# Performance work log

Hardware: AMD Instinct MI355X
Metric: run time of the kernel (lower is better)

## Reference

```python
import jax, jax.numpy as jnp
import numpy as np
import math

# dims
B, C, T, P = 32, 8, 20000, 25          # batch, emg channels, time, patch size
D, H, M, NL = 512, 8, 256, 2            # d_model, heads, random features, layers
FFN, NC, HID = 1024, 10, 128            # ffn hidden, num classes, pool hidden
DH = D // H                             # d_head
EPS_LN = 1e-5


def _sample_omega(d, m, rng):
    # Orthogonal Random Features: blocks of QR(G) rows scaled by chi(d) norms
    blocks = []
    for _ in range(math.ceil(m / d)):
        G = rng.standard_normal((d, d)).astype(np.float32)
        Q, _ = np.linalg.qr(G)
        S = Q * np.linalg.norm(G, axis=1, keepdims=True)
        blocks.append(S.T)
    return np.concatenate(blocks, axis=1)[:, :m]


def setup_inputs() -> dict:
    key = jax.random.key(0)
    ks = jax.random.split(key, 16)
    rng = np.random.default_rng(0)
    s = 0.02
    f32 = jnp.float32
    return {
        "x": jax.random.normal(ks[0], (B, C, T), f32),
        "patch_W": jax.random.normal(ks[1], (C * P, D), f32) * s,
        "patch_b": jnp.zeros((D,), f32),
        "patch_g": jnp.ones((D,), f32),
        "patch_beta": jnp.zeros((D,), f32),
        "ln1_g": jnp.ones((NL, D), f32),
        "ln1_b": jnp.zeros((NL, D), f32),
        "qW": jax.random.normal(ks[2], (NL, D, D), f32) * s,
        "kW": jax.random.normal(ks[3], (NL, D, D), f32) * s,
        "vW": jax.random.normal(ks[4], (NL, D, D), f32) * s,
        "oW": jax.random.normal(ks[5], (NL, D, D), f32) * s,
        "ob": jnp.zeros((NL, D), f32),
        "omega": jnp.stack([jnp.asarray(_sample_omega(DH, M, rng)) for _ in range(NL)]),
        "ln2_g": jnp.ones((NL, D), f32),
        "ln2_b": jnp.zeros((NL, D), f32),
        "f1W": jax.random.normal(ks[6], (NL, D, FFN), f32) * s,
        "f1b": jnp.zeros((NL, FFN), f32),
        "f2W": jax.random.normal(ks[7], (NL, FFN, D), f32) * s,
        "f2b": jnp.zeros((NL, D), f32),
        "poolW1": jax.random.normal(ks[8], (D, HID), f32) * s,
        "poolW2": jax.random.normal(ks[9], (HID, 1), f32) * s,
        "headW": jax.random.normal(ks[10], (2 * D, NC), f32) * s,
        "headb": jnp.zeros((NC,), f32),
    }


def _ln(x, g, b):
    mu = jnp.mean(x, -1, keepdims=True)
    v = jnp.mean((x - mu) ** 2, -1, keepdims=True)
    return (x - mu) / jnp.sqrt(v + EPS_LN) * g + b


def _phi(x, omega):
    # FAVOR+ positive feature map: exp(x'w / d^{1/4} - |x|^2/(2 sqrt(d))) / sqrt(m)
    xs = x / (DH ** 0.25)                               # (B,H,L,d)
    proj = jnp.einsum('bhld,dm->bhlm', xs, omega)       # (B,H,L,m)
    nsq = 0.5 * jnp.sum(xs * xs, -1, keepdims=True)
    return jnp.exp(proj - nsq) / (M ** 0.5)


def _attn(x, qW, kW, vW, oW, ob, omega):
    Bx, L, _ = x.shape
    Q = (x @ qW).reshape(Bx, L, H, DH).transpose(0, 2, 1, 3)
    K = (x @ kW).reshape(Bx, L, H, DH).transpose(0, 2, 1, 3)
    V = (x @ vW).reshape(Bx, L, H, DH).transpose(0, 2, 1, 3)
    Qf = _phi(Q, omega)
    Kf = _phi(K, omega)
    KV = jnp.einsum('bhlm,bhld->bhmd', Kf, V)           # O(L m d)
    out = jnp.einsum('bhlm,bhmd->bhld', Qf, KV)
    norm = jnp.einsum('bhlm,bhm->bhl', Qf, Kf.sum(2))[..., None]
    out = out / jnp.maximum(norm, 1e-6)
    out = out.transpose(0, 2, 1, 3).reshape(Bx, L, D)
    return out @ oW + ob


def _forward(x, patch_W, patch_b, patch_g, patch_beta, ln1_g, ln1_b, qW, kW, vW,
             oW, ob, omega, ln2_g, ln2_b, f1W, f1b, f2W, f2b, poolW1, poolW2,
             headW, headb):
    Bx, Cx, Tx = x.shape
    pad = (-Tx) % P
    if pad:
        x = jnp.pad(x, ((0, 0), (0, 0), (0, pad)))
    L = x.shape[2] // P
    # patchify: (B,C,T)->(B,L,C*P) then linear + LN
    tok = x.reshape(Bx, Cx, L, P).transpose(0, 2, 1, 3).reshape(Bx, L, Cx * P)
    h = _ln(tok @ patch_W + patch_b, patch_g, patch_beta)
    for l in range(NL):  # pre-LN performer layers (dropout = eval mode)
        h = h + _attn(_ln(h, ln1_g[l], ln1_b[l]), qW[l], kW[l], vW[l], oW[l], ob[l], omega[l])
        z = _ln(h, ln2_g[l], ln2_b[l])
        h = h + (jax.nn.gelu(z @ f1W[l] + f1b[l], approximate=False) @ f2W[l] + f2b[l])
    # attentive statistics pooling over tokens
    alpha = jax.nn.softmax(jnp.tanh(h @ poolW1) @ poolW2, axis=1)  # (B,L,1)
    mu = jnp.sum(alpha * h, axis=1)
    var = jnp.sum(alpha * h * h, axis=1) - mu * mu
    feat = jnp.concatenate([mu, jnp.sqrt(jnp.clip(var, 1e-8))], axis=1)
    return feat @ headW + headb  # (B, NC)


def reference(x, patch_W, patch_b, patch_g, patch_beta, ln1_g, ln1_b, qW, kW, vW,
              oW, ob, omega, ln2_g, ln2_b, f1W, f1b, f2W, f2b, poolW1, poolW2,
              headW, headb):
    return _forward(x, patch_W, patch_b, patch_g, patch_beta, ln1_g, ln1_b, qW,
                    kW, vW, oW, ob, omega, ln2_g, ln2_b, f1W, f1b, f2W, f2b,
                    poolW1, poolW2, headW, headb)
```

## Files before the change

kernel.cpp:

```cpp
#include <hip/hip_runtime.h>
#include <math.h>

#define BB 32
#define CC 8
#define TT 20000
#define PP 25
#define LL 800
#define CP 200
#define DD 512
#define HH 8
#define MM 256
#define NLAYER 2
#define DHH 64
#define FF 1024
#define NCLS 10
#define HIDP 128
#define BL (BB*LL)
#define KPATCH 256

#define WT_PATCH 0
#define WT_QKV0  131072
#define WT_OW0   917504
#define WT_F10   1179648
#define WT_F20   1703936
#define WT_QKV1  2228224
#define WT_OW1   3014656
#define WT_F11   3276800
#define WT_F21   3801088
#define WT_POOL  4325376
#define WT_TOTAL 4390912
#define NUC 5120

typedef unsigned short u16;
typedef unsigned int u32;
typedef __attribute__((ext_vector_type(8))) short short8;
typedef __attribute__((ext_vector_type(4))) float f32x4;

__device__ __forceinline__ float b2f(u16 v) { return __uint_as_float(((u32)v) << 16); }
__device__ __forceinline__ float b2f_lo(u32 u) { return __uint_as_float(u << 16); }
__device__ __forceinline__ float b2f_hi(u32 u) { return __uint_as_float(u & 0xFFFF0000u); }
__device__ __forceinline__ u16 f2b(float f) {
  u32 u = __float_as_uint(f);
  u32 r = u + 0x7FFFu + ((u >> 16) & 1u);
  return (u16)(r >> 16);
}
__device__ __forceinline__ float ldx(const void* p, size_t i, int flag) {
  return flag ? b2f(((const u16*)p)[i]) : ((const float*)p)[i];
}
typedef const __attribute__((address_space(1))) u32 gas_u32;
typedef __attribute__((address_space(3))) u32 las_u32;
__device__ __forceinline__ void gload16(const void* g, void* l) {
  __builtin_amdgcn_global_load_lds((gas_u32*)(size_t)g, (las_u32*)(size_t)l, 16, 0, 0);
}

__global__ void sniff_kernel(const u32* __restrict__ g, u32* __restrict__ flagp) {
  if (threadIdx.x == 0) flagp[0] = (g[0] == 0x3F800000u) ? 0u : 1u;
}

__global__ void sentinel_kernel(u16* out, int n) {
  int i = blockIdx.x * 256 + threadIdx.x;
  if (i < n) out[i] = f2b(1.0e9f);
}

__global__ void patchify_kernel(const void* __restrict__ x, u16* __restrict__ tok,
                                const u32* __restrict__ dflag) {
  int flag = (int)dflag[0];
  int idx = blockIdx.x * 256 + threadIdx.x;
  if (idx >= BL * KPATCH) return;
  int col = idx & (KPATCH - 1), row = idx >> 8;
  if (col >= CP) { tok[idx] = 0; return; }
  int b = row / LL, l = row % LL;
  int c = col / PP, p = col % PP;
  tok[idx] = f2b(ldx(x, ((size_t)b * CC + c) * TT + l * PP + p, flag));
}

__global__ void omcvt_kernel(const void* __restrict__ om, u16* __restrict__ ombT,
                             const u32* __restrict__ dflag) {
  int flag = (int)dflag[0];
  const float inv4 = 0.35355339059327373f;
  int idx = blockIdx.x * 256 + threadIdx.x;
  if (idx >= NLAYER * MM * DHH) return;
  int l = idx >> 14;
  int r = idx & (MM * DHH - 1);
  int feat = r >> 6, k = r & 63;
  ombT[idx] = f2b(inv4 * ldx(om, (size_t)l * DHH * MM + (size_t)k * MM + feat, flag));
}

struct Seg { int t0, wsel, gsel, woff, goff, wtoff, ucoff, K, N, Kp; };
__constant__ Seg g_segs[14] = {
  {   0, 0, -1,      0,   0, WT_PATCH,          -1,  200,  512,  256},
  {  32, 2,  0,      0,   0, WT_QKV0,             0,  512,  512,  512},
  {  96, 3,  0,      0,   0, WT_QKV0 + 262144,  512,  512,  512,  512},
  { 160, 1,  0,      0,   0, WT_QKV0 + 524288, 1024,  512,  512,  512},
  { 224, 4, -1,      0,   0, WT_OW0,            -1,  512,  512,  512},
  { 288, 5,  1,      0,   0, WT_F10,           1536,  512, 1024,  512},
  { 416, 6, -1,      0,   0, WT_F20,            -1, 1024,  512, 1024},
  { 544, 2,  0, 262144, 512, WT_QKV1,          2560,  512,  512,  512},
  { 608, 3,  0, 262144, 512, WT_QKV1 + 262144, 3072,  512,  512,  512},
  { 672, 1,  0, 262144, 512, WT_QKV1 + 524288, 3584,  512,  512,  512},
  { 736, 4, -1, 262144,   0, WT_OW1,            -1,  512,  512,  512},
  { 800, 5,  1, 524288, 512, WT_F11,           4096,  512, 1024,  512},
  { 928, 6, -1, 524288,   0, WT_F21,            -1, 1024,  512, 1024},
  {1056, 7, -1,      0,   0, WT_POOL,           -1,  512,  128,  512},
};

__global__ __launch_bounds__(256) void megawt_kernel(
    const void* __restrict__ patchW, const void* __restrict__ qW,
    const void* __restrict__ kW, const void* __restrict__ vW,
    const void* __restrict__ oW, const void* __restrict__ f1W,
    const void* __restrict__ f2W, const void* __restrict__ poolW1,
    const void* __restrict__ ln1g, const void* __restrict__ ln1b,
    const void* __restrict__ ln2g, const void* __restrict__ ln2b,
    u16* __restrict__ wtall, float* __restrict__ pU, float* __restrict__ pC,
    const u32* __restrict__ dflag) {
  int flag = (int)dflag[0];
  int bid = blockIdx.x;
  int si = 0;
#pragma unroll
  for (int i = 1; i < 14; i++) if (bid >= g_segs[i].t0) si = i;
  Seg sg = g_segs[si];
  const void* W = (sg.wsel == 0) ? patchW : (sg.wsel == 1) ? qW : (sg.wsel == 2) ? kW
               : (sg.wsel == 3) ? vW : (sg.wsel == 4) ? oW : (sg.wsel == 5) ? f1W
               : (sg.wsel == 6) ? f2W : poolW1;
  const void* gv = (sg.gsel == 0) ? ln1g : (sg.gsel == 1) ? ln2g : nullptr;
  const void* bv = (sg.gsel == 0) ? ln1b : (sg.gsel == 1) ? ln2b : nullptr;
  int lt = bid - sg.t0;
  int nx = sg.N >> 6;
  int n0 = (lt % nx) * 64, k0 = (lt / nx) * 64;
  bool hasU = sg.ucoff >= 0;

  __shared__ float tile[64][65];
  __shared__ float sU[4][64], sC[4][64];
  int tn = threadIdx.x & 63;
  int tk = threadIdx.x >> 6;
  float su = 0.f, sc = 0.f;
#pragma unroll 4
  for (int i = 0; i < 16; i++) {
    int k = k0 + tk * 16 + i;
    float gw = 0.f;
    if (k < sg.K) {
      float w = ldx(W, (size_t)sg.woff + (size_t)k * sg.N + n0 + tn, flag);
      float g = gv ? ldx(gv, (size_t)sg.goff + k, flag) : 1.0f;
      gw = g * w;
      if (hasU) {
        su += gw;
        sc = fmaf(ldx(bv, (size_t)sg.goff + k, flag), w, sc);
      }
    }
    tile[tk * 16 + i][tn] = gw;
  }
  if (hasU) { sU[tk][tn] = su; sC[tk][tn] = sc; }
  __syncthreads();
  if (hasU && tk == 0) {
    pU[(size_t)(k0 >> 6) * NUC + sg.ucoff + n0 + tn] =
        sU[0][tn] + sU[1][tn] + sU[2][tn] + sU[3][tn];
    pC[(size_t)(k0 >> 6) * NUC + sg.ucoff + n0 + tn] =
        sC[0][tn] + sC[1][tn] + sC[2][tn] + sC[3][tn];
  }
#pragma unroll 4
  for (int i = 0; i < 16; i++) {
    int n = n0 + tk * 16 + i;
    wtall[(size_t)sg.wtoff + (size_t)n * sg.Kp + k0 + tn] = f2b(tile[tn][tk * 16 + i]);
  }
}

__global__ __launch_bounds__(256) void ucr_kernel(const float* __restrict__ pU,
    const float* __restrict__ pC, float* __restrict__ u, float* __restrict__ c, int N) {
  int n = blockIdx.x * 256 + threadIdx.x;
  if (n >= N) return;
  float su = 0.f, sc = 0.f;
#pragma unroll
  for (int ky = 0; ky < 8; ky++) {
    su += pU[(size_t)ky * N + n];
    sc += pC[(size_t)ky * N + n];
  }
  u[n] = su;
  c[n] = sc;
}

template<int ACT, bool HAS_BIAS, bool HAS_RES, int LNE, bool SPLIT3, bool STATS, bool SCORE>
__global__ __launch_bounds__(256, 4) void mgemm(
    const u16* __restrict__ A, const u16* __restrict__ Wt,
    const void* __restrict__ bias, size_t biasoff,
    const float* __restrict__ stA, const float* __restrict__ stB,
    const float* __restrict__ uvec, const float* __restrict__ cvec,
    const u16* res, u16* out, u16* out2, u16* out3,
    float* __restrict__ oSum, float* __restrict__ oSsq,
    int Kp, int N, const u32* __restrict__ dflag) {
  const int flag = (int)dflag[0];
  alignas(16) __shared__ u16 smem[128 * 128];
  __shared__ float statL[256];
  u16* As = smem;
  u16* Bs = smem + 128 * 64;
  int tid = threadIdx.x;
  int flat = blockIdx.y * gridDim.x + blockIdx.x;
  int xcd = flat & 7;
  int p_ = flat >> 3;
  int gx = gridDim.x;
  int mtile = xcd * (gridDim.y >> 3) + p_ / gx;
  int ntile = p_ % gx;
  int m0 = mtile * 128, n0 = ntile * 128;
  int wid = tid >> 6, lane = tid & 63;
  int wm = (wid >> 1) * 64, wn = (wid & 1) * 64;
  int quad = lane >> 4, cl = lane & 15;

  if (LNE == 1) {
    if (tid < 128) {
      statL[tid] = stA[m0 + tid];
      statL[128 + tid] = stB[m0 + tid];
    }
  } else if (LNE == 2) {
    if (tid < 128) {
      float s = 0.f, q = 0.f;
#pragma unroll
      for (int s8 = 0; s8 < 8; s8++) {
        s += stA[(size_t)s8 * BL + m0 + tid];
        q += stB[(size_t)s8 * BL + m0 + tid];
      }
      float mu = s * (1.f / DD);
      float var = q * (1.f / DD) - mu * mu;
      statL[tid] = mu;
      statL[128 + tid] = 1.0f / sqrtf(var + 1e-5f);
    }
  }

  f32x4 acc[4][4] = {};
  int r_ = tid >> 3, c_ = tid & 7;
  for (int k0 = 0; k0 < Kp; k0 += 64) {
    __syncthreads();
#pragma unroll
    for (int p = 0; p < 4; p++) {
      int row = p * 32 + r_;
      int gc = (c_ ^ (row & 7)) * 8;
      int lbase = ((p * 256 + (tid & ~63)) * 8);
      gload16(A + (size_t)(m0 + row) * Kp + k0 + gc, &As[lbase]);
      gload16(Wt + (size_t)(n0 + row) * Kp + k0 + gc, &Bs[lbase]);
    }
    __syncthreads();
#pragma unroll
    for (int kk = 0; kk < 64; kk += 32) {
      int qb = (kk >> 3) + quad;
      short8 af[4], bf[4];
#pragma unroll
      for (int mt = 0; mt < 4; mt++) {
        int arow = wm + mt * 16 + cl;
        af[mt] = *(const short8*)(&As[(arow * 8 + (qb ^ (cl & 7))) * 8]);
      }
#pragma unroll
      for (int nt = 0; nt < 4; nt++) {
        int brow = wn + nt * 16 + cl;
        bf[nt] = *(const short8*)(&Bs[(brow * 8 + (qb ^ (cl & 7))) * 8]);
      }
#pragma unroll
      for (int mt = 0; mt < 4; mt++)
#pragma unroll
        for (int nt = 0; nt < 4; nt++)
          acc[mt][nt] = __builtin_amdgcn_mfma_f32_16x16x32_bf16(
              af[mt], bf[nt], acc[mt][nt], 0, 0, 0);
    }
  }
  __syncthreads();
  u16* Cs = smem;
  float sA[4][4] = {}, qA[4][4] = {};
#pragma unroll
  for (int nt = 0; nt < 4; nt++) {
    int tcol = wn + nt * 16 + cl;
    int gcol = n0 + tcol;
    float bvv = HAS_BIAS ? ldx(bias, biasoff + gcol, flag) : 0.f;
    float uv_ = 0.f, cv_ = 0.f;
    if (LNE) { uv_ = uvec[gcol]; cv_ = cvec[gcol]; }
#pragma unroll
    for (int mt = 0; mt < 4; mt++) {
#pragma unroll
      for (int r = 0; r < 4; r++) {
        int trow = wm + mt * 16 + quad * 4 + r;
        int grow = m0 + trow;
        float v = acc[mt][nt][r];
        if (LNE) {
          float rv_ = statL[128 + trow];
          v = rv_ * v - rv_ * statL[trow] * uv_ + cv_;
        }
        v += bvv;
        if (ACT == 1) v = 0.5f * v * (1.0f + erff(v * 0.7071067811865476f));
        else if (ACT == 2) v = tanhf(v);
        if (HAS_RES) v += b2f(res[(size_t)grow * N + gcol]);
        u16 wv = f2b(v);
        Cs[trow * 128 + tcol] = wv;
        if (STATS) {
          float vr = b2f(wv);
          sA[mt][r] += vr;
          qA[mt][r] += vr * vr;
        }
      }
    }
  }
  if (STATS) {
#pragma unroll
    for (int mt = 0; mt < 4; mt++)
#pragma unroll
      for (int r = 0; r < 4; r++) {
        float s = sA[mt][r], q = qA[mt][r];
        s += __shfl_xor(s, 1, 64); s += __shfl_xor(s, 2, 64);
        s += __shfl_xor(s, 4, 64); s += __shfl_xor(s, 8, 64);
        q += __shfl_xor(q, 1, 64); q += __shfl_xor(q, 2, 64);
        q += __shfl_xor(q, 4, 64); q += __shfl_xor(q, 8, 64);
        if (cl == 0) {
          int grow = m0 + wm + mt * 16 + quad * 4 + r;
          int slot = ntile * 2 + (wid & 1);
          oSum[(size_t)slot * BL + grow] = s;
          oSsq[(size_t)slot * BL + grow] = q;
        }
      }
  }
  __syncthreads();
  if (SCORE) {
    int row = tid >> 1, half = tid & 1;
    float p = 0.f;
#pragma unroll
    for (int j = 0; j < 64; j++) {
      int col = (half << 6) | ((j + row) & 63);
      p += b2f(Cs[row * 128 + col]) * ldx(bias, col, flag);
    }
    p += __shfl_xor(p, 1, 64);
    if (half == 0) oSum[m0 + row] = p;
  } else {
    u16* dstbuf;
    int colbase, stride;
    if (SPLIT3) {
      int sel = n0 >> 9;
      dstbuf = (sel == 0) ? out : (sel == 1) ? out2 : out3;
      colbase = n0 & 511;
      stride = 512;
    } else {
      dstbuf = out;
      colbase = n0;
      stride = N;
    }
    int c8 = (tid & 15) * 8, rb = tid >> 4;
#pragma unroll
    for (int i = 0; i < 8; i++) {
      int trow = i * 16 + rb;
      uint4 vv = *(const uint4*)(&Cs[trow * 128 + c8]);
      *(uint4*)(&dstbuf[(size_t)(m0 + trow) * stride + colbase + c8]) = vv;
    }
  }
}

__global__ __launch_bounds__(256) void ln_apply_kernel(const u16* __restrict__ x,
    const float* __restrict__ pSum, const float* __restrict__ pSsq,
    const void* __restrict__ g, const void* __restrict__ b, u16* __restrict__ out,
    float* __restrict__ muv, float* __restrict__ rinvv,
    const u32* __restrict__ dflag) {
  int flag = (int)dflag[0];
  int row = blockIdx.x * 4 + (threadIdx.x >> 6);
  int lane = threadIdx.x & 63;
  float s = 0.f, q = 0.f;
#pragma unroll
  for (int s8 = 0; s8 < 8; s8++) {
    s += pSum[(size_t)s8 * BL + row];
    q += pSsq[(size_t)s8 * BL + row];
  }
  float m = s * (1.f / DD);
  float var = q * (1.f / DD) - m * m;
  float rvv = 1.0f / sqrtf(var + 1e-5f);

  const u16* xr = x + (size_t)row * DD + lane * 8;
  uint4 u = *(const uint4*)xr;
  float f[8] = {b2f_lo(u.x), b2f_hi(u.x), b2f_lo(u.y), b2f_hi(u.y),
                b2f_lo(u.z), b2f_hi(u.z), b2f_lo(u.w), b2f_hi(u.w)};
  u16 r[8];
  float os = 0.f, oq = 0.f;
#pragma unroll
  for (int j = 0; j < 8; j++) {
    float gg = ldx(g, lane * 8 + j, flag);
    float bb = ldx(b, lane * 8 + j, flag);
    r[j] = f2b((f[j] - m) * rvv * gg + bb);
    float hv = b2f(r[j]);
    os += hv;
    oq = fmaf(hv, hv, oq);
  }
  uint4 pr;
  pr.x = (u32)r[0] | ((u32)r[1] << 16);
  pr.y = (u32)r[2] | ((u32)r[3] << 16);
  pr.z = (u32)r[4] | ((u32)r[5] << 16);
  pr.w = (u32)r[6] | ((u32)r[7] << 16);
  *(uint4*)(out + (size_t)row * DD + lane * 8) = pr;
#pragma unroll
  for (int o = 1; o < 64; o <<= 1) {
    os += __shfl_xor(os, o, 64);
    oq += __shfl_xor(oq, o, 64);
  }
  if (lane == 0) {
    float mo = os * (1.f / DD);
    float vo = oq * (1.f / DD) - mo * mo;
    muv[row] = mo;
    rinvv[row] = 1.0f / sqrtf(vo + 1e-5f);
  }
}

__global__ __launch_bounds__(256) void kv_kernel_mfma(
    const u16* __restrict__ Kb, const u16* __restrict__ Vb,
    const u16* __restrict__ omt, u16* __restrict__ KVT_g) {
  int bh = blockIdx.x; int b = bh >> 3, h = bh & 7;
  int tid = threadIdx.x;
  int wid = tid >> 6, lane = tid & 63;
  int quad = lane >> 4, cl = lane & 15;
  __shared__ u16 VT[80 * 40];
  __shared__ u16 KfT[256 * 40];

  short8 omB[4][2];
#pragma unroll
  for (int nt = 0; nt < 4; nt++)
#pragma unroll
    for (int ks = 0; ks < 2; ks++)
      omB[nt][ks] = *(const short8*)(omt + (size_t)(wid * 64 + nt * 16 + cl) * 64
                                         + ks * 32 + quad * 8);
  for (int e = tid; e < 512; e += 256)
    VT[(64 + (e >> 5)) * 40 + (e & 31)] = ((e >> 5) == 0) ? (u16)0x3F80 : (u16)0;

  u32 vreg[4];
#pragma unroll
  for (int i = 0; i < 4; i++) {
    int idx = tid + i * 256;
    int rr = idx >> 5, pp = idx & 31;
    vreg[i] = *(const u32*)(Vb + ((size_t)(b * LL + rr)) * DD + h * DHH + pp * 2);
  }

  f32x4 acc2[4][5] = {};

  for (int l0 = 0; l0 < LL; l0 += 32) {
    __syncthreads();
#pragma unroll
    for (int i = 0; i < 4; i++) {
      int idx = tid + i * 256;
      int rr = idx >> 5, pp = idx & 31;
      u32 uv = vreg[i];
      VT[(pp * 2) * 40 + rr] = (u16)(uv & 0xFFFF);
      VT[(pp * 2 + 1) * 40 + rr] = (u16)(uv >> 16);
    }
    if (l0 + 32 < LL) {
#pragma unroll
      for (int i = 0; i < 4; i++) {
        int idx = tid + i * 256;
        int rr = idx >> 5, pp = idx & 31;
        vreg[i] = *(const u32*)(Vb + ((size_t)(b * LL + l0 + 32 + rr)) * DD
                                 + h * DHH + pp * 2);
      }
    }
    short8 aK[2][2];
    float nsk[2];
#pragma unroll
    for (int mt = 0; mt < 2; mt++) {
      const u16* ksrc = Kb + ((size_t)(b * LL + l0 + mt * 16 + cl)) * DD + h * DHH;
#pragma unroll
      for (int ks = 0; ks < 2; ks++)
        aK[mt][ks] = *(const short8*)(ksrc + ks * 32 + quad * 8);
      float q = 0.f;
#pragma unroll
      for (int ks = 0; ks < 2; ks++)
#pragma unroll
        for (int j = 0; j < 8; j++) {
          float f = b2f((u16)aK[mt][ks][j]);
          q = fmaf(f, f, q);
        }
      q += __shfl_xor(q, 16, 64);
      q += __shfl_xor(q, 32, 64);
      nsk[mt] = 0.0625f * q;
    }
    f32x4 acc1[2][4] = {};
#pragma unroll
    for (int ks = 0; ks < 2; ks++)
#pragma unroll
      for (int mt = 0; mt < 2; mt++)
#pragma unroll
        for (int nt = 0; nt < 4; nt++)
          acc1[mt][nt] = __builtin_amdgcn_mfma_f32_16x16x32_bf16(
              aK[mt][ks], omB[nt][ks], acc1[mt][nt], 0, 0, 0);
#pragma unroll
    for (int mt = 0; mt < 2; mt++) {
      f32x4 nsv;
#pragma unroll
      for (int r = 0; r < 4; r++) nsv[r] = __shfl(nsk[mt], quad * 4 + r, 64);
#pragma unroll
      for (int nt = 0; nt < 4; nt++) {
        int m = wid * 64 + nt * 16 + cl;
        u16 kf16[4];
#pragma unroll
        for (int r = 0; r < 4; r++)
          kf16[r] = f2b(__expf(acc1[mt][nt][r] - nsv[r]) * 0.0625f);
        uint2 pk;
        pk.x = (u32)kf16[0] | ((u32)kf16[1] << 16);
        pk.y = (u32)kf16[2] | ((u32)kf16[3] << 16);
        *(uint2*)(&KfT[m * 40 + mt * 16 + quad * 4]) = pk;
      }
    }
    __syncthreads();
    short8 aF[4], bV[5];
#pragma unroll
    for (int mt2 = 0; mt2 < 4; mt2++)
      aF[mt2] = *(const short8*)(&KfT[(wid * 64 + mt2 * 16 + cl) * 40 + quad * 8]);
#pragma unroll
    for (int nt2 = 0; nt2 < 5; nt2++)
      bV[nt2] = *(const short8*)(&VT[(nt2 * 16 + cl) * 40 + quad * 8]);
#pragma unroll
    for (int mt2 = 0; mt2 < 4; mt2++)
#pragma unroll
      for (int nt2 = 0; nt2 < 5; nt2++)
        acc2[mt2][nt2] = __builtin_amdgcn_mfma_f32_16x16x32_bf16(
            aF[mt2], bV[nt2], acc2[mt2][nt2], 0, 0, 0);
  }
  u16* base = KVT_g + (size_t)bh * 80 * 256;
#pragma unroll
  for (int mt2 = 0; mt2 < 4; mt2++) {
    int m0 = wid * 64 + mt2 * 16 + quad * 4;
#pragma unroll
    for (int nt2 = 0; nt2 < 4; nt2++) {
      u16 w[4];
#pragma unroll
      for (int r = 0; r < 4; r++) w[r] = f2b(acc2[mt2][nt2][r]);
      uint2 pk;
      pk.x = (u32)w[0] | ((u32)w[1] << 16);
      pk.y = (u32)w[2] | ((u32)w[3] << 16);
      *(uint2*)(&base[(size_t)(nt2 * 16 + cl) * 256 + m0]) = pk;
    }
    if (cl == 0) {
      u16 w[4];
#pragma unroll
      for (int r = 0; r < 4; r++) w[r] = f2b(acc2[mt2][4][r]);
      uint2 pk;
      pk.x = (u32)w[0] | ((u32)w[1] << 16);
      pk.y = (u32)w[2] | ((u32)w[3] << 16);
      *(uint2*)(&base[(size_t)64 * 256 + m0]) = pk;
    }
  }
}

__global__ __launch_bounds__(256) void attn_out_mfma(
    u16* __restrict__ Qb, const u16* __restrict__ KVT_g,
    const u16* __restrict__ omt) {
  int bh = blockIdx.x; int b = bh >> 3, h = bh & 7;
  int chunk = blockIdx.y;
  int tid = threadIdx.x;
  int wid = tid >> 6, lane = tid & 63;
  int quad = lane >> 4, cl = lane & 15;
  __shared__ u16 smem[64 * 264 + 80 * 264];
  u16* Qf = smem;
  u16* KVT = smem + 64 * 264;

  const u16* kvsrc = KVT_g + (size_t)bh * 80 * 256;
#pragma unroll
  for (int i = 0; i < 9; i++) {
    int idx = tid + i * 256;
    if (idx < 2080) {
      int row = idx >> 5, c8 = (idx & 31) * 8;
      *(uint4*)(&KVT[row * 264 + c8]) = *(const uint4*)(kvsrc + (size_t)row * 256 + c8);
    }
  }

  short8 omB[4][2];
#pragma unroll
  for (int nt = 0; nt < 4; nt++)
#pragma unroll
    for (int ks = 0; ks < 2; ks++)
      omB[nt][ks] = *(const short8*)(omt + (size_t)(wid * 64 + nt * 16 + cl) * 64
                                         + ks * 32 + quad * 8);

  int t0 = chunk * 64;
  short8 aQ[4][2];
  float nss[4];
#pragma unroll
  for (int mt = 0; mt < 4; mt++) {
    int tglob = t0 + mt * 16 + cl;
    int trow = tglob < LL ? tglob : LL - 1;
    const u16* qsrc = Qb + ((size_t)(b * LL + trow)) * DD + h * DHH;
#pragma unroll
    for (int ks = 0; ks < 2; ks++)
      aQ[mt][ks] = *(const short8*)(qsrc + ks * 32 + quad * 8);
    float q = 0.f;
#pragma unroll
    for (int ks = 0; ks < 2; ks++)
#pragma unroll
      for (int j = 0; j < 8; j++) {
        float f = b2f((u16)aQ[mt][ks][j]);
        q = fmaf(f, f, q);
      }
    q += __shfl_xor(q, 16, 64);
    q += __shfl_xor(q, 32, 64);
    nss[mt] = 0.0625f * q;
  }

  f32x4 acc1[4][4] = {};
#pragma unroll
  for (int ks = 0; ks < 2; ks++)
#pragma unroll
    for (int mt = 0; mt < 4; mt++)
#pragma unroll
      for (int nt = 0; nt < 4; nt++)
        acc1[mt][nt] = __builtin_amdgcn_mfma_f32_16x16x32_bf16(
            omB[nt][ks], aQ[mt][ks], acc1[mt][nt], 0, 0, 0);
#pragma unroll
  for (int mt = 0; mt < 4; mt++) {
#pragma unroll
    for (int nt = 0; nt < 4; nt++) {
      u16 w[4];
#pragma unroll
      for (int r = 0; r < 4; r++)
        w[r] = f2b(__expf(acc1[mt][nt][r] - nss[mt]) * 0.0625f);
      uint2 pk;
      pk.x = (u32)w[0] | ((u32)w[1] << 16);
      pk.y = (u32)w[2] | ((u32)w[3] << 16);
      *(uint2*)(&Qf[(mt * 16 + cl) * 264 + wid * 64 + nt * 16 + quad * 4]) = pk;
    }
  }
  __syncthreads();
  f32x4 acc2[5] = {};
#pragma unroll
  for (int ks2 = 0; ks2 < 8; ks2++) {
    short8 aF = *(const short8*)(&Qf[(wid * 16 + cl) * 264 + ks2 * 32 + quad * 8]);
#pragma unroll
    for (int nt2 = 0; nt2 < 5; nt2++) {
      short8 bK = *(const short8*)(&KVT[(nt2 * 16 + cl) * 264 + ks2 * 32 + quad * 8]);
      acc2[nt2] = __builtin_amdgcn_mfma_f32_16x16x32_bf16(bK, aF, acc2[nt2], 0, 0, 0);
    }
  }
  float nval = __shfl(acc2[4][0], cl, 64);
  float inv = 1.0f / fmaxf(nval, 1e-6f);
  int tglob = t0 + wid * 16 + cl;
  if (tglob < LL) {
    u16* dst = Qb + ((size_t)(b * LL + tglob)) * DD + h * DHH;
#pragma unroll
    for (int nt2 = 0; nt2 < 4; nt2++) {
      u16 w[4];
#pragma unroll
      for (int r = 0; r < 4; r++) w[r] = f2b(acc2[nt2][r] * inv);
      uint2 pk;
      pk.x = (u32)w[0] | ((u32)w[1] << 16);
      pk.y = (u32)w[2] | ((u32)w[3] << 16);
      *(uint2*)(dst + nt2 * 16 + quad * 4) = pk;
    }
  }
}

__global__ __launch_bounds__(256) void softmax_kernel(const float* __restrict__ sc,
    float* __restrict__ alpha) {
  __shared__ float sm[4];
  int b = blockIdx.x, tid = threadIdx.x;
  float mx = -1e30f;
  for (int i = tid; i < LL; i += 256) mx = fmaxf(mx, sc[b * LL + i]);
#pragma unroll
  for (int o = 32; o; o >>= 1) mx = fmaxf(mx, __shfl_down(mx, o, 64));
  if ((tid & 63) == 0) sm[tid >> 6] = mx;
  __syncthreads();
  mx = fmaxf(fmaxf(sm[0], sm[1]), fmaxf(sm[2], sm[3]));
  float s = 0.f;
  for (int i = tid; i < LL; i += 256) {
    float e = expf(sc[b * LL + i] - mx);
    alpha[b * LL + i] = e;
    s += e;
  }
  __syncthreads();
#pragma unroll
  for (int o = 32; o; o >>= 1) s += __shfl_down(s, o, 64);
  if ((tid & 63) == 0) sm[tid >> 6] = s;
  __syncthreads();
  float invs = 1.f / (sm[0] + sm[1] + sm[2] + sm[3]);
  for (int i = tid; i < LL; i += 256) alpha[b * LL + i] *= invs;
}

__global__ __launch_bounds__(512) void pool_part_kernel(const u16* __restrict__ h,
    const float* __restrict__ alpha, float* __restrict__ pmu, float* __restrict__ pm2) {
  int b = blockIdx.x, seg = blockIdx.y, d = threadIdx.x;
  const u16* hb = h + (size_t)b * LL * DD + (size_t)seg * 100 * DD + d;
  const float* ab = alpha + b * LL + seg * 100;
  float mu = 0.f, m2 = 0.f;
  for (int l = 0; l < 100; l++) {
    float a = ab[l], v = b2f(hb[(size_t)l * DD]);
    mu = fmaf(a, v, mu);
    m2 = fmaf(a * v, v, m2);
  }
  pmu[((size_t)seg * BB + b) * DD + d] = mu;
  pm2[((size_t)seg * BB + b) * DD + d] = m2;
}

__global__ __launch_bounds__(512) void pool_reduce_kernel(const float* __restrict__ pmu,
    const float* __restrict__ pm2, float* __restrict__ feat) {
  int b = blockIdx.x, d = threadIdx.x;
  float mu = 0.f, m2 = 0.f;
#pragma unroll
  for (int s = 0; s < 8; s++) {
    mu += pmu[((size_t)s * BB + b) * DD + d];
    m2 += pm2[((size_t)s * BB + b) * DD + d];
  }
  feat[b * 2 * DD + d] = mu;
  feat[b * 2 * DD + DD + d] = sqrtf(fmaxf(m2 - mu * mu, 1e-8f));
}

__global__ __launch_bounds__(320) void head_kernel(const float* __restrict__ feat,
    const void* __restrict__ hw, const void* __restrict__ hb, void* out,
    const u32* __restrict__ dflag) {
  int flag = (int)dflag[0];
  int b = blockIdx.x;
  int t = threadIdx.x;
  int n = t >> 5, j0 = t & 31;
  float p = 0.f;
  for (int j = j0; j < 2 * DD; j += 32)
    p = fmaf(feat[b * 2 * DD + j], ldx(hw, (size_t)j * NCLS + n, flag), p);
#pragma unroll
  for (int o = 16; o; o >>= 1) p += __shfl_down(p, o, 32);
  if (j0 == 0) {
    float v = p + ldx(hb, n, flag);
    if (flag) ((u16*)out)[b * NCLS + n] = f2b(v);
    else ((float*)out)[b * NCLS + n] = v;
  }
}

extern "C" void kernel_launch(void* const* d_in, const int* in_sizes, int n_in,
                              void* d_out, int out_size, void* d_ws, size_t ws_size,
                              hipStream_t stream) {
  char* ws = (char*)d_ws;
  size_t off = 0;
  auto alloc = [&](size_t bytes) -> char* {
    char* p = ws + off;
    off += (bytes + 255) & ~(size_t)255;
    return p;
  };
  u16* hbuf = (u16*)alloc((size_t)BL * DD * 2);
  u16* buf1 = (u16*)alloc((size_t)BL * DD * 2);
  u16* buf2 = (u16*)alloc((size_t)BL * DD * 2);
  u16* KVT_g = (u16*)alloc((size_t)BB * HH * 80 * 256 * 2);
  float* muv = (float*)alloc((size_t)BL * 4);
  float* rinvv = (float*)alloc((size_t)BL * 4);
  float* scores = (float*)alloc((size_t)BL * 4);
  float* alpha = (float*)alloc((size_t)BL * 4);
  float* feat = (float*)alloc((size_t)BB * 2 * DD * 4);
  float* uvec = (float*)alloc((size_t)NUC * 4);
  float* cvec = (float*)alloc((size_t)NUC * 4);
  float* pU = (float*)alloc((size_t)8 * NUC * 4);
  float* pC = (float*)alloc((size_t)8 * NUC * 4);
  float* pSum = (float*)alloc((size_t)8 * BL * 4);
  float* pSsq = (float*)alloc((size_t)8 * BL * 4);
  u16* ombT = (u16*)alloc((size_t)NLAYER * MM * DHH * 2);
  u16* wtall = (u16*)alloc((size_t)WT_TOTAL * 2);
  u32* dflag = (u32*)alloc(256);
  size_t off_base = off;
  u16* bufQ = (u16*)alloc((size_t)BL * DD * 2);
  size_t off_full = off;

  if (ws_size < off_base) {
    sentinel_kernel<<<2, 256, 0, stream>>>((u16*)d_out, out_size);
    return;
  }
  const bool fused = (ws_size >= off_full);

  const void* x       = d_in[0];
  const void* patchW  = d_in[1];
  const void* patchb  = d_in[2];
  const void* patchg  = d_in[3];
  const void* patchbe = d_in[4];
  const void* ln1g    = d_in[5];
  const void* ln1b    = d_in[6];
  const void* qW      = d_in[7];
  const void* kW      = d_in[8];
  const void* vW      = d_in[9];
  const void* oW      = d_in[10];
  const void* ob      = d_in[11];
  const void* omg     = d_in[12];
  const void* ln2g    = d_in[13];
  const void* ln2b    = d_in[14];
  const void* f1W     = d_in[15];
  const void* f1b     = d_in[16];
  const void* f2W     = d_in[17];
  const void* f2b_    = d_in[18];
  const void* poolW1  = d_in[19];
  const void* poolW2  = d_in[20];
  const void* headW   = d_in[21];
  const void* headb   = d_in[22];

  sniff_kernel<<<1, 64, 0, stream>>>((const u32*)patchg, dflag);

  patchify_kernel<<<(BL * KPATCH) / 256, 256, 0, stream>>>(x, buf1, dflag);
  omcvt_kernel<<<(NLAYER * MM * DHH + 255) / 256, 256, 0, stream>>>(omg, ombT, dflag);
  megawt_kernel<<<1072, 256, 0, stream>>>(patchW, qW, kW, vW, oW, f1W, f2W, poolW1,
                                          ln1g, ln1b, ln2g, ln2b, wtall, pU, pC, dflag);
  ucr_kernel<<<NUC / 256, 256, 0, stream>>>(pU, pC, uvec, cvec, NUC);

  mgemm<0, true, false, 0, false, true, false><<<dim3(4, 200), 256, 0, stream>>>(
      buf1, wtall + WT_PATCH, patchb, 0, nullptr, nullptr, nullptr, nullptr,
      nullptr, buf2, nullptr, nullptr, pSum, pSsq, KPATCH, DD, dflag);
  ln_apply_kernel<<<BL / 4, 256, 0, stream>>>(buf2, pSum, pSsq, patchg, patchbe,
                                              hbuf, muv, rinvv, dflag);

  for (int l = 0; l < NLAYER; l++) {
    size_t oD = (size_t)l * DD;
    size_t oF = (size_t)l * FF;
    const u16* omtl = ombT + (size_t)l * MM * DHH;
    const u16* qkvT = wtall + (l == 0 ? WT_QKV0 : WT_QKV1);
    const u16* oWT  = wtall + (l == 0 ? WT_OW0 : WT_OW1);
    const u16* f1T  = wtall + (l == 0 ? WT_F10 : WT_F11);
    const u16* f2T  = wtall + (l == 0 ? WT_F20 : WT_F21);
    const float* uq = uvec + (l == 0 ? 0 : 2560);
    const float* cq = cvec + (l == 0 ? 0 : 2560);
    const float* uf = uvec + (l == 0 ? 1536 : 4096);
    const float* cf = cvec + (l == 0 ? 1536 : 4096);

    u16* qb;
    if (fused) {
      if (l == 0)
        mgemm<0, false, false, 1, true, false, false><<<dim3(12, 200), 256, 0, stream>>>(
            hbuf, qkvT, nullptr, 0, muv, rinvv, uq, cq, nullptr,
            buf1, buf2, bufQ, nullptr, nullptr, DD, 3 * DD, dflag);
      else
        mgemm<0, false, false, 2, true, false, false><<<dim3(12, 200), 256, 0, stream>>>(
            hbuf, qkvT, nullptr, 0, pSum, pSsq, uq, cq, nullptr,
            buf1, buf2, bufQ, nullptr, nullptr, DD, 3 * DD, dflag);
      kv_kernel_mfma<<<BB * HH, 256, 0, stream>>>(buf1, buf2, omtl, KVT_g);
      qb = bufQ;
    } else {
      if (l == 0) {
        mgemm<0, false, false, 1, false, false, false><<<dim3(4, 200), 256, 0, stream>>>(
            hbuf, qkvT, nullptr, 0, muv, rinvv, uq, cq, nullptr,
            buf1, nullptr, nullptr, nullptr, nullptr, DD, DD, dflag);
        mgemm<0, false, false, 1, false, false, false><<<dim3(4, 200), 256, 0, stream>>>(
            hbuf, qkvT + 262144, nullptr, 0, muv, rinvv, uq + 512, cq + 512, nullptr,
            buf2, nullptr, nullptr, nullptr, nullptr, DD, DD, dflag);
      } else {
        mgemm<0, false, false, 2, false, false, false><<<dim3(4, 200), 256, 0, stream>>>(
            hbuf, qkvT, nullptr, 0, pSum, pSsq, uq, cq, nullptr,
            buf1, nullptr, nullptr, nullptr, nullptr, DD, DD, dflag);
        mgemm<0, false, false, 2, false, false, false><<<dim3(4, 200), 256, 0, stream>>>(
            hbuf, qkvT + 262144, nullptr, 0, pSum, pSsq, uq + 512, cq + 512, nullptr,
            buf2, nullptr, nullptr, nullptr, nullptr, DD, DD, dflag);
      }
      kv_kernel_mfma<<<BB * HH, 256, 0, stream>>>(buf1, buf2, omtl, KVT_g);
      if (l == 0)
        mgemm<0, false, false, 1, false, false, false><<<dim3(4, 200), 256, 0, stream>>>(
            hbuf, qkvT + 524288, nullptr, 0, muv, rinvv, uq + 1024, cq + 1024, nullptr,
            buf1, nullptr, nullptr, nullptr, nullptr, DD, DD, dflag);
      else
        mgemm<0, false, false, 2, false, false, false><<<dim3(4, 200), 256, 0, stream>>>(
            hbuf, qkvT + 524288, nullptr, 0, pSum, pSsq, uq + 1024, cq + 1024, nullptr,
            buf1, nullptr, nullptr, nullptr, nullptr, DD, DD, dflag);
      qb = buf1;
    }
    attn_out_mfma<<<dim3(BB * HH, 13), 256, 0, stream>>>(qb, KVT_g, omtl);
    mgemm<0, true, true, 0, false, true, false><<<dim3(4, 200), 256, 0, stream>>>(
        qb, oWT, ob, oD, nullptr, nullptr, nullptr, nullptr,
        hbuf, hbuf, nullptr, nullptr, pSum, pSsq, DD, DD, dflag);
    mgemm<1, true, false, 2, false, false, false><<<dim3(8, 200), 256, 0, stream>>>(
        hbuf, f1T, f1b, oF, pSum, pSsq, uf, cf, nullptr,
        buf1, nullptr, nullptr, nullptr, nullptr, DD, FF, dflag);
    if (l == 0)
      mgemm<0, true, true, 0, false, true, false><<<dim3(4, 200), 256, 0, stream>>>(
          buf1, f2T, f2b_, oD, nullptr, nullptr, nullptr, nullptr,
          hbuf, hbuf, nullptr, nullptr, pSum, pSsq, FF, DD, dflag);
    else
      mgemm<0, true, true, 0, false, false, false><<<dim3(4, 200), 256, 0, stream>>>(
          buf1, f2T, f2b_, oD, nullptr, nullptr, nullptr, nullptr,
          hbuf, hbuf, nullptr, nullptr, nullptr, nullptr, FF, DD, dflag);
  }

  mgemm<2, false, false, 0, false, false, true><<<dim3(1, 200), 256, 0, stream>>>(
      hbuf, wtall + WT_POOL, poolW2, 0, nullptr, nullptr, nullptr, nullptr,
      nullptr, nullptr, nullptr, nullptr, scores, nullptr, DD, HIDP, dflag);
  softmax_kernel<<<BB, 256, 0, stream>>>(scores, alpha);
  pool_part_kernel<<<dim3(BB, 8), 512, 0, stream>>>(hbuf, alpha, pSum, pSsq);
  pool_reduce_kernel<<<BB, 512, 0, stream>>>(pSum, pSsq, feat);
  head_kernel<<<BB, 320, 0, stream>>>(feat, headW, headb, d_out, dflag);
}
```

Measured before the change: 987.8 us.

## Split kv_kernel sequence across two wave groups with 512-thread blocks

The K-feature/V outer-product kernel now runs 512 threads per (batch, head) block. Two groups of four waves each process alternating 32-token chunks, so each loop iteration covers 64 tokens and the serial loop has half as many iterations. Each group keeps its own shared-memory VT/KfT buffers. The two groups' accumulators are reduced through shared memory at the end. The aim is more parallelism per block for a grid of only 256 blocks, at the cost of doubled LDS use, an extra reduction phase, and an idle group on the final partial chunk.

Result: faster. 813.1 us (-17.7%).

```diff
diff --git a/kernel.cpp b/kernel.cpp
--- a/kernel.cpp
+++ b/kernel.cpp
@@ -398,139 +398,174 @@
   }
 }
 
-__global__ __launch_bounds__(256) void kv_kernel_mfma(
+__global__ __launch_bounds__(512) void kv_kernel_mfma(
     const u16* __restrict__ Kb, const u16* __restrict__ Vb,
     const u16* __restrict__ omt, u16* __restrict__ KVT_g) {
   int bh = blockIdx.x; int b = bh >> 3, h = bh & 7;
   int tid = threadIdx.x;
-  int wid = tid >> 6, lane = tid & 63;
+  int wid = tid >> 6;
+  int g = wid >> 2;
+  int w4 = wid & 3;
+  int lane = tid & 63;
   int quad = lane >> 4, cl = lane & 15;
-  __shared__ u16 VT[80 * 40];
-  __shared__ u16 KfT[256 * 40];
+  alignas(16) __shared__ u16 VT[2][80 * 40];
+  alignas(16) __shared__ u16 KfT[2][256 * 40];
 
   short8 omB[4][2];
 #pragma unroll
   for (int nt = 0; nt < 4; nt++)
 #pragma unroll
     for (int ks = 0; ks < 2; ks++)
-      omB[nt][ks] = *(const short8*)(omt + (size_t)(wid * 64 + nt * 16 + cl) * 64
+      omB[nt][ks] = *(const short8*)(omt + (size_t)(w4 * 64 + nt * 16 + cl) * 64
                                          + ks * 32 + quad * 8);
-  for (int e = tid; e < 512; e += 256)
-    VT[(64 + (e >> 5)) * 40 + (e & 31)] = ((e >> 5) == 0) ? (u16)0x3F80 : (u16)0;
+  for (int e = tid; e < 1024; e += 512) {
+    int gg = e >> 9, r = (e >> 5) & 15, c = e & 31;
+    VT[gg][(64 + r) * 40 + c] = (r == 0) ? (u16)0x3F80 : (u16)0;
+  }
 
   u32 vreg[4];
 #pragma unroll
   for (int i = 0; i < 4; i++) {
-    int idx = tid + i * 256;
+    int idx = tid + i * 512;
     int rr = idx >> 5, pp = idx & 31;
     vreg[i] = *(const u32*)(Vb + ((size_t)(b * LL + rr)) * DD + h * DHH + pp * 2);
   }
 
   f32x4 acc2[4][5] = {};
 
-  for (int l0 = 0; l0 < LL; l0 += 32) {
+  for (int l0 = 0; l0 < LL; l0 += 64) {
     __syncthreads();
 #pragma unroll
     for (int i = 0; i < 4; i++) {
-      int idx = tid + i * 256;
+      int idx = tid + i * 512;
       int rr = idx >> 5, pp = idx & 31;
       u32 uv = vreg[i];
-      VT[(pp * 2) * 40 + rr] = (u16)(uv & 0xFFFF);
-      VT[(pp * 2 + 1) * 40 + rr] = (u16)(uv >> 16);
-    }
-    if (l0 + 32 < LL) {
+      u16* vt = &VT[rr >> 5][0];
+      int rl = rr & 31;
+      vt[(pp * 2) * 40 + rl] = (u16)(uv & 0xFFFF);
+      vt[(pp * 2 + 1) * 40 + rl] = (u16)(uv >> 16);
+    }
+    if (l0 + 64 < LL) {
 #pragma unroll
       for (int i = 0; i < 4; i++) {
-        int idx = tid + i * 256;
+        int idx = tid + i * 512;
         int rr = idx >> 5, pp = idx & 31;
-        vreg[i] = *(const u32*)(Vb + ((size_t)(b * LL + l0 + 32 + rr)) * DD
-                                 + h * DHH + pp * 2);
-      }
-    }
-    short8 aK[2][2];
-    float nsk[2];
-#pragma unroll
-    for (int mt = 0; mt < 2; mt++) {
-      const u16* ksrc = Kb + ((size_t)(b * LL + l0 + mt * 16 + cl)) * DD + h * DHH;
+        int row = l0 + 64 + rr;
+        if (row < LL)
+          vreg[i] = *(const u32*)(Vb + ((size_t)(b * LL + row)) * DD + h * DHH + pp * 2);
+      }
+    }
+    int myl0 = l0 + g * 32;
+    bool act = myl0 < LL;
+    if (act) {
+      short8 aK[2][2];
+      float nsk[2];
+#pragma unroll
+      for (int mt = 0; mt < 2; mt++) {
+        const u16* ksrc = Kb + ((size_t)(b * LL + myl0 + mt * 16 + cl)) * DD + h * DHH;
+#pragma unroll
+        for (int ks = 0; ks < 2; ks++)
+          aK[mt][ks] = *(const short8*)(ksrc + ks * 32 + quad * 8);
+        float q = 0.f;
+#pragma unroll
+        for (int ks = 0; ks < 2; ks++)
+#pragma unroll
+          for (int j = 0; j < 8; j++) {
+            float f = b2f((u16)aK[mt][ks][j]);
+            q = fmaf(f, f, q);
+          }
+        q += __shfl_xor(q, 16, 64);
+        q += __shfl_xor(q, 32, 64);
+        nsk[mt] = 0.0625f * q;
+      }
+      f32x4 acc1[2][4] = {};
 #pragma unroll
       for (int ks = 0; ks < 2; ks++)
-        aK[mt][ks] = *(const short8*)(ksrc + ks * 32 + quad * 8);
-      float q = 0.f;
-#pragma unroll
-      for (int ks = 0; ks < 2; ks++)
-#pragma unroll
-        for (int j = 0; j < 8; j++) {
-          float f = b2f((u16)aK[mt][ks][j]);
-          q = fmaf(f, f, q);
+#pragma unroll
+        for (int mt = 0; mt < 2; mt++)
+#pragma unroll
+          for (int nt = 0; nt < 4; nt++)
+            acc1[mt][nt] = __builtin_amdgcn_mfma_f32_16x16x32_bf16(
+                aK[mt][ks], omB[nt][ks], acc1[mt][nt], 0, 0, 0);
+#pragma unroll
+      for (int mt = 0; mt < 2; mt++) {
+        f32x4 nsv;
+#pragma unroll
+        for (int r = 0; r < 4; r++) nsv[r] = __shfl(nsk[mt], quad * 4 + r, 64);
+#pragma unroll
+        for (int nt = 0; nt < 4; nt++) {
+          int m = w4 * 64 + nt * 16 + cl;
+          u16 kf16[4];
+#pragma unroll
+          for (int r = 0; r < 4; r++)
+            kf16[r] = f2b(__expf(acc1[mt][nt][r] - nsv[r]) * 0.0625f);
+          uint2 pk;
+          pk.x = (u32)kf16[0] | ((u32)kf16[1] << 16);
+          pk.y = (u32)kf16[2] | ((u32)kf16[3] << 16);
+          *(uint2*)(&KfT[g][m * 40 + mt * 16 + quad * 4]) = pk;
         }
-      q += __shfl_xor(q, 16, 64);
-      q += __shfl_xor(q, 32, 64);
-      nsk[mt] = 0.0625f * q;
-    }
-    f32x4 acc1[2][4] = {};
-#pragma unroll
-    for (int ks = 0; ks < 2; ks++)
-#pragma unroll
-      for (int mt = 0; mt < 2; mt++)
-#pragma unroll
-        for (int nt = 0; nt < 4; nt++)
-          acc1[mt][nt] = __builtin_amdgcn_mfma_f32_16x16x32_bf16(
-              aK[mt][ks], omB[nt][ks], acc1[mt][nt], 0, 0, 0);
-#pragma unroll
-    for (int mt = 0; mt < 2; mt++) {
-      f32x4 nsv;
-#pragma unroll
-      for (int r = 0; r < 4; r++) nsv[r] = __shfl(nsk[mt], quad * 4 + r, 64);
-#pragma unroll
-      for (int nt = 0; nt < 4; nt++) {
-        int m = wid * 64 + nt * 16 + cl;
-        u16 kf16[4];
-#pragma unroll
-        for (int r = 0; r < 4; r++)
-          kf16[r] = f2b(__expf(acc1[mt][nt][r] - nsv[r]) * 0.0625f);
+      }
+    }
+    __syncthreads();
+    if (act) {
+      short8 aF[4], bV[5];
+#pragma unroll
+      for (int mt2 = 0; mt2 < 4; mt2++)
+        aF[mt2] = *(const short8*)(&KfT[g][(w4 * 64 + mt2 * 16 + cl) * 40 + quad * 8]);
+#pragma unroll
+      for (int nt2 = 0; nt2 < 5; nt2++)
+        bV[nt2] = *(const short8*)(&VT[g][(nt2 * 16 + cl) * 40 + quad * 8]);
+#pragma unroll
+      for (int mt2 = 0; mt2 < 4; mt2++)
+#pragma unroll
+        for (int nt2 = 0; nt2 < 5; nt2++)
+          acc2[mt2][nt2] = __builtin_amdgcn_mfma_f32_16x16x32_bf16(
+              aF[mt2], bV[nt2], acc2[mt2][nt2], 0, 0, 0);
+    }
+  }
+  float* stg = (float*)&KfT[0][0];
+#pragma unroll
+  for (int mt2 = 0; mt2 < 4; mt2++) {
+    __syncthreads();
+    if (g == 1) {
+#pragma unroll
+      for (int nt2 = 0; nt2 < 5; nt2++)
+        *(f32x4*)&stg[((w4 * 5 + nt2) * 64 + lane) * 4] = acc2[mt2][nt2];
+    }
+    __syncthreads();
+    if (g == 0) {
+#pragma unroll
+      for (int nt2 = 0; nt2 < 5; nt2++) {
+        f32x4 o = *(const f32x4*)&stg[((w4 * 5 + nt2) * 64 + lane) * 4];
+#pragma unroll
+        for (int r = 0; r < 4; r++) acc2[mt2][nt2][r] += o[r];
+      }
+    }
+  }
+  if (g == 0) {
+    u16* base = KVT_g + (size_t)bh * 80 * 256;
+#pragma unroll
+    for (int mt2 = 0; mt2 < 4; mt2++) {
+      int m0 = w4 * 64 + mt2 * 16 + quad * 4;
+#pragma unroll
+      for (int nt2 = 0; nt2 < 4; nt2++) {
+        u16 w[4];
+#pragma unroll
+        for (int r = 0; r < 4; r++) w[r] = f2b(acc2[mt2][nt2][r]);
         uint2 pk;
-        pk.x = (u32)kf16[0] | ((u32)kf16[1] << 16);
-        pk.y = (u32)kf16[2] | ((u32)kf16[3] << 16);
-        *(uint2*)(&KfT[m * 40 + mt * 16 + quad * 4]) = pk;
-      }
-    }
-    __syncthreads();
-    short8 aF[4], bV[5];
-#pragma unroll
-    for (int mt2 = 0; mt2 < 4; mt2++)
-      aF[mt2] = *(const short8*)(&KfT[(wid * 64 + mt2 * 16 + cl) * 40 + quad * 8]);
-#pragma unroll
-    for (int nt2 = 0; nt2 < 5; nt2++)
-      bV[nt2] = *(const short8*)(&VT[(nt2 * 16 + cl) * 40 + quad * 8]);
-#pragma unroll
-    for (int mt2 = 0; mt2 < 4; mt2++)
-#pragma unroll
-      for (int nt2 = 0; nt2 < 5; nt2++)
-        acc2[mt2][nt2] = __builtin_amdgcn_mfma_f32_16x16x32_bf16(
-            aF[mt2], bV[nt2], acc2[mt2][nt2], 0, 0, 0);
-  }
-  u16* base = KVT_g + (size_t)bh * 80 * 256;
-#pragma unroll
-  for (int mt2 = 0; mt2 < 4; mt2++) {
-    int m0 = wid * 64 + mt2 * 16 + quad * 4;
-#pragma unroll
-    for (int nt2 = 0; nt2 < 4; nt2++) {
-      u16 w[4];
-#pragma unroll
-      for (int r = 0; r < 4; r++) w[r] = f2b(acc2[mt2][nt2][r]);
-      uint2 pk;
-      pk.x = (u32)w[0] | ((u32)w[1] << 16);
-      pk.y = (u32)w[2] | ((u32)w[3] << 16);
-      *(uint2*)(&base[(size_t)(nt2 * 16 + cl) * 256 + m0]) = pk;
-    }
-    if (cl == 0) {
-      u16 w[4];
-#pragma unroll
-      for (int r = 0; r < 4; r++) w[r] = f2b(acc2[mt2][4][r]);
-      uint2 pk;
-      pk.x = (u32)w[0] | ((u32)w[1] << 16);
-      pk.y = (u32)w[2] | ((u32)w[3] << 16);
-      *(uint2*)(&base[(size_t)64 * 256 + m0]) = pk;
+        pk.x = (u32)w[0] | ((u32)w[1] << 16);
+        pk.y = (u32)w[2] | ((u32)w[3] << 16);
+        *(uint2*)(&base[(size_t)(nt2 * 16 + cl) * 256 + m0]) = pk;
+      }
+      if (cl == 0) {
+        u16 w[4];
+#pragma unroll
+        for (int r = 0; r < 4; r++) w[r] = f2b(acc2[mt2][4][r]);
+        uint2 pk;
+        pk.x = (u32)w[0] | ((u32)w[1] << 16);
+        pk.y = (u32)w[2] | ((u32)w[3] << 16);
+        *(uint2*)(&base[(size_t)64 * 256 + m0]) = pk;
+      }
     }
   }
 }
@@ -813,7 +848,7 @@
         mgemm<0, false, false, 2, true, false, false><<<dim3(12, 200), 256, 0, stream>>>(
             hbuf, qkvT, nullptr, 0, pSum, pSsq, uq, cq, nullptr,
             buf1, buf2, bufQ, nullptr, nullptr, DD, 3 * DD, dflag);
-      kv_kernel_mfma<<<BB * HH, 256, 0, stream>>>(buf1, buf2, omtl, KVT_g);
+      kv_kernel_mfma<<<BB * HH, 512, 0, stream>>>(buf1, buf2, omtl, KVT_g);
       qb = bufQ;
     } else {
       if (l == 0) {
@@ -831,7 +866,7 @@
             hbuf, qkvT + 262144, nullptr, 0, pSum, pSsq, uq + 512, cq + 512, nullptr,
             buf2, nullptr, nullptr, nullptr, nullptr, DD, DD, dflag);
       }
-      kv_kernel_mfma<<<BB * HH, 256, 0, stream>>>(buf1, buf2, omtl, KVT_g);
+      kv_kernel_mfma<<<BB * HH, 512, 0, stream>>>(buf1, buf2, omtl, KVT_g);
       if (l == 0)
         mgemm<0, false, false, 1, false, false, false><<<dim3(4, 200), 256, 0, stream>>>(
             hbuf, qkvT + 524288, nullptr, 0, muv, rinvv, uq + 1024, cq + 1024, nullptr,
```
